# Optimization experiments

Hardware: AMD Instinct MI355X
Metric: run time of the kernel (lower is better)

The kernel has to match this reference:

```python
import jax, jax.numpy as jnp
import numpy as np

N_HEADS = 12


def setup_inputs() -> dict:
    key = jax.random.key(0)
    ks = jax.random.split(key, 3)
    B, N, C = 32, 1024, 768
    x = jax.random.normal(ks[0], (B, N, C), dtype=jnp.float32)
    w_qkv = jax.random.normal(ks[1], (C, 3 * C), dtype=jnp.float32) * (1.0 / np.sqrt(C))
    b_qkv = jnp.zeros((3 * C,), dtype=jnp.float32)
    w_out = jax.random.normal(ks[2], (C, C), dtype=jnp.float32) * (1.0 / np.sqrt(C))
    b_out = jnp.zeros((C,), dtype=jnp.float32)
    return {"x": x, "w_qkv": w_qkv, "b_qkv": b_qkv, "w_out": w_out, "b_out": b_out}


def reference(x, w_qkv, b_qkv, w_out, b_out):
    B, N, C = x.shape
    H = N_HEADS
    D = C // H  # head_dim
    qkv = (x @ w_qkv + b_qkv).reshape(B, N, 3, H, D)
    qkv = jnp.transpose(qkv, (2, 0, 3, 1, 4))
    q, k, v = qkv[0], qkv[1], qkv[2]
    # channel attention: k^T @ v -> (B,H,D,D), scaled by sqrt(head_dim)
    attn = jnp.einsum("bhnd,bhne->bhde", k, v) / np.sqrt(D).astype(np.float32)
    attn = jax.nn.softmax(attn, axis=-1)
    # attn @ q^T -> (B,H,D,N); swapaxes -> (B,H,N,D)
    out = jnp.einsum("bhde,bhne->bhnd", attn, q)
    # ProjOut: merge heads (B,N,C) + Dense(C)
    out = jnp.transpose(out, (0, 2, 1, 3)).reshape(B, N, C)
    return out @ w_out + b_out
```

## Files before the change

kernel.cpp:

```cpp
#include <hip/hip_runtime.h>
#include <hip/hip_bf16.h>
#include <stdint.h>
#include <stddef.h>

#define B_ 32
#define N_ 1024
#define C_ 768
#define H_ 12
#define D_ 64
#define M_ (B_*N_)
#define TC_ (3*C_)

typedef __bf16 bf16_t;
typedef __attribute__((ext_vector_type(8))) __bf16 bf16x8;
typedef __attribute__((ext_vector_type(4))) __bf16 bf16x4;
typedef __attribute__((ext_vector_type(4))) float  f32x4;

#define MFMA16(a,b,c) __builtin_amdgcn_mfma_f32_16x16x32_bf16(a,b,c,0,0,0)

__device__ __forceinline__ void lds_load16(const void* g, void* l) {
  __builtin_amdgcn_global_load_lds(
      (const __attribute__((address_space(1))) void*)g,
      (__attribute__((address_space(3))) void*)l, 16, 0, 0);
}

__global__ void cvt_bf16(const float* __restrict__ in, bf16_t* __restrict__ out, int n) {
  int i = (blockIdx.x * 256 + threadIdx.x) * 8;
  if (i >= n) return;
  const float4 a = *(const float4*)(in + i);
  const float4 b = *(const float4*)(in + i + 4);
  bf16x8 r;
  r[0]=(bf16_t)a.x; r[1]=(bf16_t)a.y; r[2]=(bf16_t)a.z; r[3]=(bf16_t)a.w;
  r[4]=(bf16_t)b.x; r[5]=(bf16_t)b.y; r[6]=(bf16_t)b.z; r[7]=(bf16_t)b.w;
  *(bf16x8*)(out + i) = r;
}

__global__ void transpose_cvt(const float* __restrict__ in, bf16_t* __restrict__ out,
                              int R, int Cc) {
  __shared__ float t[32][33];
  const int c0 = blockIdx.x * 32, r0 = blockIdx.y * 32;
  const int tx = threadIdx.x & 31, ty = threadIdx.x >> 5;
  #pragma unroll
  for (int k = 0; k < 4; ++k)
    t[ty + k*8][tx] = in[(size_t)(r0 + ty + k*8)*Cc + c0 + tx];
  __syncthreads();
  #pragma unroll
  for (int k = 0; k < 4; ++k)
    out[(size_t)(c0 + ty + k*8)*R + r0 + tx] = (bf16_t)t[tx][ty + k*8];
}

template<int MODE>
__global__ __launch_bounds__(512, 2)
void gemm_bt(const bf16_t* __restrict__ A, const bf16_t* __restrict__ BT,
             const float* __restrict__ bias, float* __restrict__ Cout,
             bf16_t* __restrict__ qh,
             bf16_t* __restrict__ kthi, bf16_t* __restrict__ vthi,
             int nbx)
{
  __shared__ __align__(16) char smem[131072];

  const int nwg = gridDim.x;
  const int cpx = nwg >> 3;
  const int bid = blockIdx.x;
  const int swz = (bid & 7) * cpx + (bid >> 3);
  const int bx  = swz % nbx;
  const int by  = swz / nbx;

  const int tid  = threadIdx.x;
  const int wave = tid >> 6;
  const int lane = tid & 63;
  const int rowBase = by * 256;
  const int colBase = bx * 256;
  const int wr = wave >> 2;
  const int wc = wave & 3;
  const int fr = lane & 15;
  const int b   = rowBase >> 10;
  const int nn0 = rowBase & (N_ - 1);

  const int srow = tid >> 2;
  const int scol = (((tid & 3) ^ ((tid >> 3) & 3)) << 3);
  const bf16_t *Ap0, *Ap1, *Bp0, *Bp1;
  if (MODE == 3) {
    Ap0 = A + (size_t)b * (H_*N_*D_) + (size_t)(nn0 + srow) * D_ + scol;
    Ap1 = Ap0 + (size_t)128 * D_;
    const size_t bts = (size_t)b * C_ * C_;
    Bp0 = BT + bts + (size_t)(colBase + srow) * 768 + scol;
    Bp1 = Bp0 + (size_t)128 * 768;
  } else {
    Ap0 = A + (size_t)(rowBase + srow) * 768 + scol;
    Ap1 = Ap0 + (size_t)128 * 768;
    Bp0 = BT + (size_t)(colBase + srow) * 768 + scol;
    Bp1 = Bp0 + (size_t)128 * 768;
  }

  const int chxA = (((lane >> 4) ^ ((fr >> 1) & 3)) << 4);
  const int aoff = (wr*128 + fr)*64 + chxA;
  const int boff = 16384 + (wc*64 + fr)*64 + chxA;

#define RDA(BI,MM) (*(const bf16x8*)(smem + (BI)*32768 + aoff + (MM)*1024))
#define RDB(BI,NN) (*(const bf16x8*)(smem + (BI)*32768 + boff + (NN)*1024))

#define A_OFF(K0) ((MODE == 3) ? ((size_t)((K0) >> 6) << 16) + ((K0) & 32) : (size_t)(K0))

#define STAGE_A(BI, T) do {                                                   \
    const int k0_ = (T) * 32;                                                 \
    const size_t ao_ = A_OFF(k0_);                                            \
    lds_load16(Ap0 + ao_, smem + (BI)*32768 + tid*16);                        \
    lds_load16(Ap1 + ao_, smem + (BI)*32768 + 8192 + tid*16);                 \
  } while (0)

#define STAGE_B(BI, T) do {                                                   \
    const int k0_ = (T) * 32;                                                 \
    lds_load16(Bp0 + k0_, smem + (BI)*32768 + 16384 + tid*16);                \
    lds_load16(Bp1 + k0_, smem + (BI)*32768 + 24576 + tid*16);                \
  } while (0)

  f32x4 acc[8][4];
  #pragma unroll
  for (int m = 0; m < 8; ++m)
    #pragma unroll
    for (int n = 0; n < 4; ++n) acc[m][n] = f32x4{0.f,0.f,0.f,0.f};

#define MFMA_HALF(MB)                                                         \
    acc[MB+0][0]=MFMA16(a0_,b0_,acc[MB+0][0]); acc[MB+0][1]=MFMA16(a0_,b1_,acc[MB+0][1]); \
    acc[MB+0][2]=MFMA16(a0_,b2_,acc[MB+0][2]); acc[MB+0][3]=MFMA16(a0_,b3_,acc[MB+0][3]); \
    acc[MB+1][0]=MFMA16(a1_,b0_,acc[MB+1][0]); acc[MB+1][1]=MFMA16(a1_,b1_,acc[MB+1][1]); \
    acc[MB+1][2]=MFMA16(a1_,b2_,acc[MB+1][2]); acc[MB+1][3]=MFMA16(a1_,b3_,acc[MB+1][3]); \
    acc[MB+2][0]=MFMA16(a2_,b0_,acc[MB+2][0]); acc[MB+2][1]=MFMA16(a2_,b1_,acc[MB+2][1]); \
    acc[MB+2][2]=MFMA16(a2_,b2_,acc[MB+2][2]); acc[MB+2][3]=MFMA16(a2_,b3_,acc[MB+2][3]); \
    acc[MB+3][0]=MFMA16(a3_,b0_,acc[MB+3][0]); acc[MB+3][1]=MFMA16(a3_,b1_,acc[MB+3][1]); \
    acc[MB+3][2]=MFMA16(a3_,b2_,acc[MB+3][2]); acc[MB+3][3]=MFMA16(a3_,b3_,acc[MB+3][3]);

#define TILE(BI, T, DOST, VM) do {                                            \
    asm volatile("s_waitcnt vmcnt(" #VM ")" ::: "memory");                    \
    __builtin_amdgcn_sched_barrier(0);                                        \
    __builtin_amdgcn_s_barrier();                                             \
    __builtin_amdgcn_sched_barrier(0);                                        \
    if (DOST) { STAGE_A(((BI)+3)&3, (T)+3); }                                 \
    __builtin_amdgcn_sched_barrier(0);                                        \
    bf16x8 b0_=RDB(BI,0), b1_=RDB(BI,1), b2_=RDB(BI,2), b3_=RDB(BI,3);        \
    bf16x8 a0_=RDA(BI,0), a1_=RDA(BI,1), a2_=RDA(BI,2), a3_=RDA(BI,3);        \
    __builtin_amdgcn_s_setprio(1);                                            \
    MFMA_HALF(0)                                                              \
    __builtin_amdgcn_s_setprio(0);                                            \
    if (DOST) { STAGE_B(((BI)+3)&3, (T)+3); }                                 \
    __builtin_amdgcn_sched_barrier(0);                                        \
    a0_=RDA(BI,4); a1_=RDA(BI,5); a2_=RDA(BI,6); a3_=RDA(BI,7);               \
    __builtin_amdgcn_s_setprio(1);                                            \
    MFMA_HALF(4)                                                              \
    __builtin_amdgcn_s_setprio(0);                                            \
    asm volatile("s_waitcnt lgkmcnt(0)" ::: "memory");                        \
    __builtin_amdgcn_sched_barrier(0);                                        \
  } while (0)

  STAGE_A(0,0); STAGE_B(0,0);
  STAGE_A(1,1); STAGE_B(1,1);
  STAGE_A(2,2); STAGE_B(2,2);

  #pragma unroll 1
  for (int t = 0; t < 20; t += 4) {
    TILE(0, t,   1, 8);
    TILE(1, t+1, 1, 8);
    TILE(2, t+2, 1, 8);
    TILE(3, t+3, 1, 8);
  }
  TILE(0, 20, 1, 8);
  TILE(1, 21, 0, 8);
  TILE(2, 22, 0, 4);
  TILE(3, 23, 0, 0);

#undef TILE
#undef MFMA_HALF
#undef STAGE_A
#undef STAGE_B
#undef A_OFF
#undef RDA
#undef RDB

  if (MODE == 3) {
    #pragma unroll
    for (int n = 0; n < 4; ++n) {
      const int gc = colBase + wc*64 + n*16 + fr;
      const float bb = bias[gc];
      #pragma unroll
      for (int m = 0; m < 8; ++m) {
        const int gr = rowBase + wr*128 + m*16 + ((lane >> 4) << 2);
        #pragma unroll
        for (int j = 0; j < 4; ++j)
          Cout[(size_t)(gr + j)*C_ + gc] = acc[m][n][j] + bb;
      }
    }
  } else {
    __syncthreads();
    bf16_t* tile = (bf16_t*)smem;
    const int s = colBase / C_;
    #pragma unroll 1
    for (int ch = 0; ch < 4; ++ch) {
      if (ch) __syncthreads();
      if (wc == ch) {
        #pragma unroll
        for (int n = 0; n < 4; ++n) {
          const int cl = n*16 + fr;
          const float bb = bias[colBase + ch*64 + cl];
          #pragma unroll
          for (int m = 0; m < 8; ++m) {
            const int r0 = wr*128 + m*16 + ((lane >> 4) << 2);
            bf16x4 hv;
            hv[0]=(bf16_t)(acc[m][n][0]+bb); hv[1]=(bf16_t)(acc[m][n][1]+bb);
            hv[2]=(bf16_t)(acc[m][n][2]+bb); hv[3]=(bf16_t)(acc[m][n][3]+bb);
            *(bf16x4*)&tile[cl*260 + r0] = hv;
          }
        }
      }
      __syncthreads();
      const int gcol0 = colBase + ch*64;
      if (s == 0) {
        const int h = gcol0 >> 6;
        const int r = tid >> 1, hh = tid & 1;
        bf16_t* dst = qh + (((size_t)b*H_ + h)*N_ + nn0 + r)*D_ + hh*32;
        #pragma unroll
        for (int i0 = 0; i0 < 32; i0 += 8) {
          bf16x8 vv;
          #pragma unroll
          for (int i = 0; i < 8; ++i) vv[i] = tile[(hh*32 + i0 + i)*260 + r];
          *(bf16x8*)&dst[i0] = vv;
        }
      } else {
        const int rem = gcol0 - s*C_;
        const int h = rem >> 6;
        const int d = tid >> 3, nq = (tid & 7)*32;
        bf16_t* dst = (s == 1 ? kthi : vthi)
                      + (((size_t)b*H_ + h)*D_ + d)*N_ + nn0 + nq;
        #pragma unroll
        for (int i0 = 0; i0 < 32; i0 += 8)
          *(bf16x8*)&dst[i0] = *(const bf16x8*)&tile[d*260 + nq + i0];
      }
    }
  }
}

__global__ __launch_bounds__(256, 2)
void attn_softmax_k(const bf16_t* __restrict__ kthi, const bf16_t* __restrict__ vthi,
                    bf16_t* __restrict__ attnT)
{
  __shared__ float tile[64][65];
  __shared__ float invs[64];
  const int bh = blockIdx.x;
  const int tid = threadIdx.x, wave = tid >> 6, lane = tid & 63;
  const int fr = lane & 15, fo = (lane >> 4) * 8;
  const size_t base = (size_t)bh * D_ * N_;
  f32x4 acc[4][4] = {{0.f,0.f,0.f,0.f}};
  const int k0lo = wave * 256;
  #pragma unroll 1
  for (int k0 = k0lo; k0 < k0lo + 256; k0 += 32) {
    bf16x8 ah[4], bhv[4];
    #pragma unroll
    for (int m = 0; m < 4; ++m)
      ah[m] = *(const bf16x8*)&kthi[base + (size_t)(m*16 + fr)*N_ + k0 + fo];
    #pragma unroll
    for (int n = 0; n < 4; ++n)
      bhv[n] = *(const bf16x8*)&vthi[base + (size_t)(n*16 + fr)*N_ + k0 + fo];
    #pragma unroll
    for (int m = 0; m < 4; ++m)
      #pragma unroll
      for (int n = 0; n < 4; ++n)
        acc[m][n] = MFMA16(ah[m], bhv[n], acc[m][n]);
  }
  for (int w = 0; w < 4; ++w) {
    if (wave == w) {
      #pragma unroll
      for (int m = 0; m < 4; ++m)
        #pragma unroll
        for (int n = 0; n < 4; ++n) {
          const int row = m*16 + ((lane >> 4) << 2);
          const int col = n*16 + fr;
          #pragma unroll
          for (int j = 0; j < 4; ++j) {
            if (w == 0) tile[row+j][col]  = acc[m][n][j];
            else        tile[row+j][col] += acc[m][n][j];
          }
        }
    }
    __syncthreads();
  }
  if (tid < 64) {
    float mx = -3.0e38f;
    #pragma unroll
    for (int c = 0; c < 64; ++c) mx = fmaxf(mx, tile[tid][c]);
    mx *= 0.125f;
    float ssum = 0.f;
    #pragma unroll
    for (int c = 0; c < 64; ++c) {
      const float ev = __expf(tile[tid][c]*0.125f - mx);
      tile[tid][c] = ev;
      ssum += ev;
    }
    invs[tid] = 1.0f / ssum;
  }
  __syncthreads();
  if (tid < 64) {
    bf16_t* ao = attnT + (size_t)bh * D_ * D_ + tid * D_;
    #pragma unroll
    for (int d0 = 0; d0 < 64; d0 += 8) {
      bf16x8 vv;
      #pragma unroll
      for (int i = 0; i < 8; ++i) vv[i] = (bf16_t)(tile[d0+i][tid] * invs[d0+i]);
      *(bf16x8*)&ao[d0] = vv;
    }
  }
}

__global__ __launch_bounds__(256, 2)
void compose_w2(const bf16_t* __restrict__ woutT, const bf16_t* __restrict__ attnT,
                bf16_t* __restrict__ w2t)
{
  const int jb = blockIdx.x;
  const int bh = blockIdx.y;
  const int b = bh / H_, h = bh - b*H_;
  const int tid = threadIdx.x, wave = tid >> 6, lane = tid & 63;
  const int fr = lane & 15, fo = (lane >> 4) * 8;
  const bf16_t* at = attnT + (size_t)bh * D_ * D_;
  f32x4 acc[2][4] = {{0.f,0.f,0.f,0.f}};
  #pragma unroll
  for (int kk = 0; kk < 2; ++kk) {
    bf16x8 af[2], bfv[4];
    #pragma unroll
    for (int m = 0; m < 2; ++m)
      af[m] = *(const bf16x8*)&woutT[(size_t)(jb*128 + wave*32 + m*16 + fr)*C_ + h*64 + kk*32 + fo];
    #pragma unroll
    for (int n = 0; n < 4; ++n)
      bfv[n] = *(const bf16x8*)&at[(n*16 + fr)*64 + kk*32 + fo];
    #pragma unroll
    for (int m = 0; m < 2; ++m)
      #pragma unroll
      for (int n = 0; n < 4; ++n)
        acc[m][n] = MFMA16(af[m], bfv[n], acc[m][n]);
  }
  bf16_t* wb = w2t + (size_t)b * C_ * C_;
  #pragma unroll
  for (int m = 0; m < 2; ++m) {
    const int j = jb*128 + wave*32 + m*16 + ((lane >> 4) << 2);
    #pragma unroll
    for (int n = 0; n < 4; ++n) {
      const int e = n*16 + fr;
      #pragma unroll
      for (int jj = 0; jj < 4; ++jj)
        wb[(size_t)(j + jj)*C_ + h*64 + e] = (bf16_t)acc[m][n][jj];
    }
  }
}

extern "C" void kernel_launch(void* const* d_in, const int* in_sizes, int n_in,
                              void* d_out, int out_size, void* d_ws, size_t ws_size,
                              hipStream_t stream)
{
  (void)in_sizes; (void)n_in; (void)out_size;
  const float* x     = (const float*)d_in[0];
  const float* w_qkv = (const float*)d_in[1];
  const float* b_qkv = (const float*)d_in[2];
  const float* w_out = (const float*)d_in[3];
  const float* b_out = (const float*)d_in[4];
  float* out = (float*)d_out;

  const size_t sz_xb   = (size_t)M_*C_*2;
  const size_t sz_wq   = (size_t)TC_*C_*2;
  const size_t sz_wo   = (size_t)C_*C_*2;
  const size_t sz_qh   = (size_t)B_*H_*N_*D_*2;
  const size_t sz_kv   = (size_t)B_*H_*D_*N_*2;
  const size_t sz_attn = (size_t)B_*H_*D_*D_*2;

  char* p = (char*)d_ws;
  bf16_t* xb    = (bf16_t*)p; p += sz_xb;
  bf16_t* wqkvT = (bf16_t*)p; p += sz_wq;
  bf16_t* woutT = (bf16_t*)p; p += sz_wo;
  bf16_t* qh    = (bf16_t*)p; p += sz_qh;
  bf16_t* kthi  = (bf16_t*)p; p += sz_kv;
  bf16_t* vthi  = (bf16_t*)p; p += sz_kv;
  bf16_t* attnT = (bf16_t*)p; p += sz_attn;
  const size_t base_need = (size_t)(p - (char*)d_ws);
  bf16_t* w2t = xb;

  if (ws_size < base_need) return;

  cvt_bf16<<<dim3((M_*C_)/2048), 256, 0, stream>>>(x, xb, M_*C_);
  transpose_cvt<<<dim3(TC_/32, C_/32), 256, 0, stream>>>(w_qkv, wqkvT, C_, TC_);
  transpose_cvt<<<dim3(C_/32,  C_/32), 256, 0, stream>>>(w_out, woutT, C_, C_);

  gemm_bt<1><<<dim3((TC_/256)*(M_/256)), 512, 0, stream>>>(
      xb, wqkvT, b_qkv, nullptr, qh, kthi, vthi, TC_/256);

  attn_softmax_k<<<dim3(B_*H_), 256, 0, stream>>>(kthi, vthi, attnT);

  compose_w2<<<dim3(C_/128, B_*H_), 256, 0, stream>>>(woutT, attnT, w2t);

  gemm_bt<3><<<dim3((C_/256)*(M_/256)), 512, 0, stream>>>(
      qh, w2t, b_out, out, nullptr, nullptr, nullptr, C_/256);
}
```

Measured before the change: 308.7 us.

## Restructure GEMM main loop to 64-wide K tiles with double buffer and phased MFMA

Replaces the 4-stage, 32-wide-K LDS ring with two 64 KiB buffers holding 64-wide K tiles, using an 8-chunk XOR swizzle. Each tile is processed in four phases that reuse B fragments held in registers, with global-to-LDS loads interleaved across phases. The goal is fewer barriers and waits per unit of K, plus better LDS fragment reuse. In exchange it adds a barrier pair per phase, uses more registers for the held B fragments, and has shallower prefetch depth.

```diff
diff --git a/kernel.cpp b/kernel.cpp
--- a/kernel.cpp
+++ b/kernel.cpp
@@ -74,46 +74,54 @@
   const int wr = wave >> 2;
   const int wc = wave & 3;
   const int fr = lane & 15;
+  const int hi = lane >> 4;
   const int b   = rowBase >> 10;
   const int nn0 = rowBase & (N_ - 1);
 
-  const int srow = tid >> 2;
-  const int scol = (((tid & 3) ^ ((tid >> 3) & 3)) << 3);
-  const bf16_t *Ap0, *Ap1, *Bp0, *Bp1;
+  const int rls  = tid >> 3;
+  const int scol = (((tid & 7) ^ ((tid >> 3) & 7)) << 3);
+  const bf16_t *ApS0, *ApS1, *BpS0, *BpS1;
+  size_t AKT, AJS;
   if (MODE == 3) {
-    Ap0 = A + (size_t)b * (H_*N_*D_) + (size_t)(nn0 + srow) * D_ + scol;
-    Ap1 = Ap0 + (size_t)128 * D_;
-    const size_t bts = (size_t)b * C_ * C_;
-    Bp0 = BT + bts + (size_t)(colBase + srow) * 768 + scol;
-    Bp1 = Bp0 + (size_t)128 * 768;
+    const bf16_t* ab = A + (size_t)b * (H_*N_*D_);
+    ApS0 = ab + (size_t)(nn0 + rls) * D_ + scol;
+    ApS1 = ab + (size_t)(nn0 + 128 + rls) * D_ + scol;
+    AKT = (size_t)N_ * D_;  AJS = (size_t)64 * D_;
   } else {
-    Ap0 = A + (size_t)(rowBase + srow) * 768 + scol;
-    Ap1 = Ap0 + (size_t)128 * 768;
-    Bp0 = BT + (size_t)(colBase + srow) * 768 + scol;
-    Bp1 = Bp0 + (size_t)128 * 768;
-  }
-
-  const int chxA = (((lane >> 4) ^ ((fr >> 1) & 3)) << 4);
-  const int aoff = (wr*128 + fr)*64 + chxA;
-  const int boff = 16384 + (wc*64 + fr)*64 + chxA;
-
-#define RDA(BI,MM) (*(const bf16x8*)(smem + (BI)*32768 + aoff + (MM)*1024))
-#define RDB(BI,NN) (*(const bf16x8*)(smem + (BI)*32768 + boff + (NN)*1024))
-
-#define A_OFF(K0) ((MODE == 3) ? ((size_t)((K0) >> 6) << 16) + ((K0) & 32) : (size_t)(K0))
-
-#define STAGE_A(BI, T) do {                                                   \
-    const int k0_ = (T) * 32;                                                 \
-    const size_t ao_ = A_OFF(k0_);                                            \
-    lds_load16(Ap0 + ao_, smem + (BI)*32768 + tid*16);                        \
-    lds_load16(Ap1 + ao_, smem + (BI)*32768 + 8192 + tid*16);                 \
-  } while (0)
-
-#define STAGE_B(BI, T) do {                                                   \
-    const int k0_ = (T) * 32;                                                 \
-    lds_load16(Bp0 + k0_, smem + (BI)*32768 + 16384 + tid*16);                \
-    lds_load16(Bp1 + k0_, smem + (BI)*32768 + 24576 + tid*16);                \
-  } while (0)
+    ApS0 = A + (size_t)(rowBase + rls) * 768 + scol;
+    ApS1 = A + (size_t)(rowBase + 128 + rls) * 768 + scol;
+    AKT = 64;  AJS = (size_t)64 * 768;
+  }
+  const size_t bts = (MODE == 3) ? (size_t)b * C_ * C_ : 0;
+  BpS0 = BT + bts + (size_t)(colBase + rls) * 768 + scol;
+  BpS1 = BT + bts + (size_t)(colBase + 128 + rls) * 768 + scol;
+  const size_t BJS = (size_t)64 * 768;
+
+  const int axr  = fr & 7;
+  const int chx0 = ((0 + hi) ^ axr) << 4;
+  const int chx1 = ((4 + hi) ^ axr) << 4;
+  const int abase = wr*16384 + fr*128;
+  const int bbase = 32768 + (wc>>1)*16384 + ((wc&1)*64 + fr)*128;
+
+#define RA(BUF,M,KK) (*(const bf16x8*)(smem + (BUF)*65536 + abase + (M)*2048 + ((KK)?chx1:chx0)))
+#define RB(BUF,N,KK) (*(const bf16x8*)(smem + (BUF)*65536 + bbase + (N)*2048 + ((KK)?chx1:chx0)))
+
+#define SGA(BUF,H,T) do{ \
+    const bf16_t* p_ = (H) ? ApS1 : ApS0; \
+    lds_load16(p_ + (size_t)(T)*AKT,       smem + (BUF)*65536 + (H)*16384 + tid*16); \
+    lds_load16(p_ + (size_t)(T)*AKT + AJS, smem + (BUF)*65536 + (H)*16384 + 8192 + tid*16); \
+  }while(0)
+#define SGB(BUF,H,T) do{ \
+    const bf16_t* p_ = (H) ? BpS1 : BpS0; \
+    lds_load16(p_ + (size_t)(T)*64,       smem + (BUF)*65536 + 32768 + (H)*16384 + tid*16); \
+    lds_load16(p_ + (size_t)(T)*64 + BJS, smem + (BUF)*65536 + 32768 + (H)*16384 + 8192 + tid*16); \
+  }while(0)
+
+#define SBR() __builtin_amdgcn_sched_barrier(0)
+#define BARX() do{ SBR(); __builtin_amdgcn_s_barrier(); SBR(); }while(0)
+#define LG0() do{ asm volatile("s_waitcnt lgkmcnt(0)":::"memory"); SBR(); }while(0)
+#define VMW4() do{ asm volatile("s_waitcnt vmcnt(4)":::"memory"); SBR(); }while(0)
+#define VMW0() do{ asm volatile("s_waitcnt vmcnt(0)":::"memory"); SBR(); }while(0)
 
   f32x4 acc[8][4];
   #pragma unroll
@@ -121,61 +129,67 @@
     #pragma unroll
     for (int n = 0; n < 4; ++n) acc[m][n] = f32x4{0.f,0.f,0.f,0.f};
 
-#define MFMA_HALF(MB)                                                         \
-    acc[MB+0][0]=MFMA16(a0_,b0_,acc[MB+0][0]); acc[MB+0][1]=MFMA16(a0_,b1_,acc[MB+0][1]); \
-    acc[MB+0][2]=MFMA16(a0_,b2_,acc[MB+0][2]); acc[MB+0][3]=MFMA16(a0_,b3_,acc[MB+0][3]); \
-    acc[MB+1][0]=MFMA16(a1_,b0_,acc[MB+1][0]); acc[MB+1][1]=MFMA16(a1_,b1_,acc[MB+1][1]); \
-    acc[MB+1][2]=MFMA16(a1_,b2_,acc[MB+1][2]); acc[MB+1][3]=MFMA16(a1_,b3_,acc[MB+1][3]); \
-    acc[MB+2][0]=MFMA16(a2_,b0_,acc[MB+2][0]); acc[MB+2][1]=MFMA16(a2_,b1_,acc[MB+2][1]); \
-    acc[MB+2][2]=MFMA16(a2_,b2_,acc[MB+2][2]); acc[MB+2][3]=MFMA16(a2_,b3_,acc[MB+2][3]); \
-    acc[MB+3][0]=MFMA16(a3_,b0_,acc[MB+3][0]); acc[MB+3][1]=MFMA16(a3_,b1_,acc[MB+3][1]); \
-    acc[MB+3][2]=MFMA16(a3_,b2_,acc[MB+3][2]); acc[MB+3][3]=MFMA16(a3_,b3_,acc[MB+3][3]);
-
-#define TILE(BI, T, DOST, VM) do {                                            \
-    asm volatile("s_waitcnt vmcnt(" #VM ")" ::: "memory");                    \
-    __builtin_amdgcn_sched_barrier(0);                                        \
-    __builtin_amdgcn_s_barrier();                                             \
-    __builtin_amdgcn_sched_barrier(0);                                        \
-    if (DOST) { STAGE_A(((BI)+3)&3, (T)+3); }                                 \
-    __builtin_amdgcn_sched_barrier(0);                                        \
-    bf16x8 b0_=RDB(BI,0), b1_=RDB(BI,1), b2_=RDB(BI,2), b3_=RDB(BI,3);        \
-    bf16x8 a0_=RDA(BI,0), a1_=RDA(BI,1), a2_=RDA(BI,2), a3_=RDA(BI,3);        \
-    __builtin_amdgcn_s_setprio(1);                                            \
-    MFMA_HALF(0)                                                              \
-    __builtin_amdgcn_s_setprio(0);                                            \
-    if (DOST) { STAGE_B(((BI)+3)&3, (T)+3); }                                 \
-    __builtin_amdgcn_sched_barrier(0);                                        \
-    a0_=RDA(BI,4); a1_=RDA(BI,5); a2_=RDA(BI,6); a3_=RDA(BI,7);               \
-    __builtin_amdgcn_s_setprio(1);                                            \
-    MFMA_HALF(4)                                                              \
-    __builtin_amdgcn_s_setprio(0);                                            \
-    asm volatile("s_waitcnt lgkmcnt(0)" ::: "memory");                        \
-    __builtin_amdgcn_sched_barrier(0);                                        \
-  } while (0)
-
-  STAGE_A(0,0); STAGE_B(0,0);
-  STAGE_A(1,1); STAGE_B(1,1);
-  STAGE_A(2,2); STAGE_B(2,2);
+  bf16x8 bfr00, bfr01, bfr10, bfr11, bfr20, bfr21, bfr30, bfr31;
+
+#define PHASE(BUF, Q, STAGES, ENDV) do{ \
+    if ((Q) == 0) { \
+      bfr00 = RB(BUF,0,0); bfr01 = RB(BUF,0,1); \
+      bfr10 = RB(BUF,1,0); bfr11 = RB(BUF,1,1); \
+      bfr20 = RB(BUF,2,0); bfr21 = RB(BUF,2,1); \
+      bfr30 = RB(BUF,3,0); bfr31 = RB(BUF,3,1); \
+    } \
+    bf16x8 a00 = RA(BUF,2*(Q)+0,0), a01 = RA(BUF,2*(Q)+0,1); \
+    bf16x8 a10 = RA(BUF,2*(Q)+1,0), a11 = RA(BUF,2*(Q)+1,1); \
+    STAGES; \
+    BARX(); LG0(); \
+    __builtin_amdgcn_s_setprio(1); \
+    acc[2*(Q)+0][0]=MFMA16(a00,bfr00,acc[2*(Q)+0][0]); acc[2*(Q)+0][0]=MFMA16(a01,bfr01,acc[2*(Q)+0][0]); \
+    acc[2*(Q)+0][1]=MFMA16(a00,bfr10,acc[2*(Q)+0][1]); acc[2*(Q)+0][1]=MFMA16(a01,bfr11,acc[2*(Q)+0][1]); \
+    acc[2*(Q)+0][2]=MFMA16(a00,bfr20,acc[2*(Q)+0][2]); acc[2*(Q)+0][2]=MFMA16(a01,bfr21,acc[2*(Q)+0][2]); \
+    acc[2*(Q)+0][3]=MFMA16(a00,bfr30,acc[2*(Q)+0][3]); acc[2*(Q)+0][3]=MFMA16(a01,bfr31,acc[2*(Q)+0][3]); \
+    acc[2*(Q)+1][0]=MFMA16(a10,bfr00,acc[2*(Q)+1][0]); acc[2*(Q)+1][0]=MFMA16(a11,bfr01,acc[2*(Q)+1][0]); \
+    acc[2*(Q)+1][1]=MFMA16(a10,bfr10,acc[2*(Q)+1][1]); acc[2*(Q)+1][1]=MFMA16(a11,bfr11,acc[2*(Q)+1][1]); \
+    acc[2*(Q)+1][2]=MFMA16(a10,bfr20,acc[2*(Q)+1][2]); acc[2*(Q)+1][2]=MFMA16(a11,bfr21,acc[2*(Q)+1][2]); \
+    acc[2*(Q)+1][3]=MFMA16(a10,bfr30,acc[2*(Q)+1][3]); acc[2*(Q)+1][3]=MFMA16(a11,bfr31,acc[2*(Q)+1][3]); \
+    __builtin_amdgcn_s_setprio(0); SBR(); \
+    ENDV; \
+    BARX(); \
+  }while(0)
+
+  SGA(0,0,0); SGA(0,1,0); SGB(0,0,0); SGB(0,1,0); SGB(1,0,1); SGB(1,1,1);
+  VMW4(); BARX();
 
   #pragma unroll 1
-  for (int t = 0; t < 20; t += 4) {
-    TILE(0, t,   1, 8);
-    TILE(1, t+1, 1, 8);
-    TILE(2, t+2, 1, 8);
-    TILE(3, t+3, 1, 8);
-  }
-  TILE(0, 20, 1, 8);
-  TILE(1, 21, 0, 8);
-  TILE(2, 22, 0, 4);
-  TILE(3, 23, 0, 0);
-
-#undef TILE
-#undef MFMA_HALF
-#undef STAGE_A
-#undef STAGE_B
-#undef A_OFF
-#undef RDA
-#undef RDB
+  for (int i = 0; i < 5; ++i) {
+    const int t0 = 2*i;
+    PHASE(0,0, { SGA(1,0,t0+1); },                     );
+    PHASE(0,1, { SGA(1,1,t0+1); SGB(0,0,t0+2); },      );
+    PHASE(0,2, { SGB(0,1,t0+2); },                     );
+    PHASE(0,3, { },                                    VMW4());
+    PHASE(1,0, { SGA(0,0,t0+2); },                     );
+    PHASE(1,1, { SGA(0,1,t0+2); },                     );
+    PHASE(1,2, { SGB(1,0,t0+3); },                     );
+    PHASE(1,3, { SGB(1,1,t0+3); },                     VMW4());
+  }
+  PHASE(0,0, { SGA(1,0,11); },  );
+  PHASE(0,1, { SGA(1,1,11); },  );
+  PHASE(0,2, { },               );
+  PHASE(0,3, { },               VMW0());
+  PHASE(1,0, { },               );
+  PHASE(1,1, { },               );
+  PHASE(1,2, { },               );
+  PHASE(1,3, { },               );
+
+#undef PHASE
+#undef SGA
+#undef SGB
+#undef RA
+#undef RB
+#undef VMW4
+#undef VMW0
+#undef LG0
+#undef BARX
+#undef SBR
 
   if (MODE == 3) {
     #pragma unroll
```

After: 302.2 us. 1.02x faster.
